# Performance work log

Measured on AMD Instinct MI355X. Metric: run time of the kernel, lower is better.

## Reference

```python
import jax, jax.numpy as jnp
import numpy as np

N_CHARS, EMB, HID, SEQ = 256, 512, 2048, 8192


def setup_inputs() -> dict:
    key = jax.random.key(0)
    ks = jax.random.split(key, 12)
    s = 0.02
    cat = EMB + HID
    return {
        "input_seq": jax.random.randint(ks[0], (SEQ,), 0, N_CHARS, dtype=jnp.int32),
        "hidden": jnp.zeros((HID,), jnp.float32),
        "cell": jnp.zeros((HID,), jnp.float32),
        "embedding": jax.random.normal(ks[1], (N_CHARS, EMB), jnp.float32) * s,
        "Wf": jax.random.normal(ks[2], (HID, cat), jnp.float32) * s,
        "bf": jax.random.normal(ks[3], (HID,), jnp.float32) * s,
        "Wi": jax.random.normal(ks[4], (HID, cat), jnp.float32) * s,
        "bi": jax.random.normal(ks[5], (HID,), jnp.float32) * s,
        "Wo": jax.random.normal(ks[6], (HID, cat), jnp.float32) * s,
        "bo": jax.random.normal(ks[7], (HID,), jnp.float32) * s,
        "Wc": jax.random.normal(ks[8], (HID, cat), jnp.float32) * s,
        "bc": jax.random.normal(ks[9], (HID,), jnp.float32) * s,
        "Wout": jax.random.normal(ks[10], (N_CHARS, HID), jnp.float32) * s,
        "bout": jax.random.normal(ks[11], (N_CHARS,), jnp.float32) * s,
    }


def reference(input_seq, hidden, cell, embedding, Wf, bf, Wi, bi, Wo, bo, Wc, bc, Wout, bout):
    def step(carry, idx):
        h, c = carry
        x = embedding[idx]                       # [EMB]
        z = jnp.concatenate([x, h])              # [EMB+HID], order matches torch concat([i, h])
        f = jax.nn.sigmoid(Wf @ z + bf)
        i = jax.nn.sigmoid(Wi @ z + bi)
        o = jax.nn.sigmoid(Wo @ z + bo)
        c_tilde = jnp.tanh(Wc @ z + bc)
        c_new = f * c + i * c_tilde
        h_new = o * jnp.tanh(c_new)
        pred = Wout @ h_new + bout               # [N_CHARS]
        return (h_new, c_new), pred

    (h, c), outs = jax.lax.scan(step, (hidden, cell), input_seq)
    return outs, h, c  # outs: [SEQ, N_CHARS]
```

## Files before the change

### kernel.cpp

```cpp
#include <hip/hip_runtime.h>
#include <cstdint>
#include <cstddef>

#define SEQ   8192
#define EMB   512
#define HID   2048
#define NCH   256
#define CAT   (EMB + HID)
#define NBLK  256
#define NTH   512
#define NROW  8192

typedef unsigned int u32x4 __attribute__((ext_vector_type(4)));

__device__ __forceinline__ unsigned long long packpair(float v, unsigned tag) {
    return ((unsigned long long)tag << 32) | (unsigned long long)__float_as_uint(v);
}

__device__ __forceinline__ float fast_sig(float x) {
    return __builtin_amdgcn_rcpf(1.f + __expf(-x));
}
__device__ __forceinline__ float fast_tanh(float x) {
    return 1.f - 2.f * __builtin_amdgcn_rcpf(__expf(2.f * x) + 1.f);
}

#define DPP_ADD(x, ctrl) \
    x += __int_as_float(__builtin_amdgcn_update_dpp(0, __float_as_int(x), ctrl, 0xF, 0xF, true))

__device__ __forceinline__ float wave_sum(float x) {
    DPP_ADD(x, 0x111);
    DPP_ADD(x, 0x112);
    DPP_ADD(x, 0x114);
    DPP_ADD(x, 0x118);
    x += __shfl_xor(x, 16, 64);
    x += __shfl_xor(x, 32, 64);
    return x;
}

#define ST4(N0,N1,N2,N3, V) asm volatile( \
    "v_accvgpr_write_b32 a" #N0 ", %0\n\t" \
    "v_accvgpr_write_b32 a" #N1 ", %1\n\t" \
    "v_accvgpr_write_b32 a" #N2 ", %2\n\t" \
    "v_accvgpr_write_b32 a" #N3 ", %3" \
    :: "v"((V).x), "v"((V).y), "v"((V).z), "v"((V).w) \
    : "a" #N0, "a" #N1, "a" #N2, "a" #N3)

#define DOT16(A0,A1,A2,A3, B0,B1,B2,B3, C0,C1,C2,C3, D0,D1,D2,D3, Z0,Z1,Z2,Z3) \
    "v_accvgpr_read_b32 v68, a" #A0 "\n\t" \
    "v_accvgpr_read_b32 v69, a" #B0 "\n\t" \
    "v_accvgpr_read_b32 v70, a" #C0 "\n\t" \
    "v_accvgpr_read_b32 v71, a" #D0 "\n\t" \
    "v_fmac_f32 %0, v68, " Z0 "\n\t" \
    "v_accvgpr_read_b32 v68, a" #A1 "\n\t" \
    "v_fmac_f32 %1, v69, " Z0 "\n\t" \
    "v_accvgpr_read_b32 v69, a" #B1 "\n\t" \
    "v_fmac_f32 %2, v70, " Z0 "\n\t" \
    "v_accvgpr_read_b32 v70, a" #C1 "\n\t" \
    "v_fmac_f32 %3, v71, " Z0 "\n\t" \
    "v_accvgpr_read_b32 v71, a" #D1 "\n\t" \
    "v_fmac_f32 %0, v68, " Z1 "\n\t" \
    "v_accvgpr_read_b32 v68, a" #A2 "\n\t" \
    "v_fmac_f32 %1, v69, " Z1 "\n\t" \
    "v_accvgpr_read_b32 v69, a" #B2 "\n\t" \
    "v_fmac_f32 %2, v70, " Z1 "\n\t" \
    "v_accvgpr_read_b32 v70, a" #C2 "\n\t" \
    "v_fmac_f32 %3, v71, " Z1 "\n\t" \
    "v_accvgpr_read_b32 v71, a" #D2 "\n\t" \
    "v_fmac_f32 %0, v68, " Z2 "\n\t" \
    "v_accvgpr_read_b32 v68, a" #A3 "\n\t" \
    "v_fmac_f32 %1, v69, " Z2 "\n\t" \
    "v_accvgpr_read_b32 v69, a" #B3 "\n\t" \
    "v_fmac_f32 %2, v70, " Z2 "\n\t" \
    "v_accvgpr_read_b32 v70, a" #C3 "\n\t" \
    "v_fmac_f32 %3, v71, " Z2 "\n\t" \
    "v_accvgpr_read_b32 v71, a" #D3 "\n\t" \
    "v_fmac_f32 %0, v68, " Z3 "\n\t" \
    "v_fmac_f32 %1, v69, " Z3 "\n\t" \
    "v_fmac_f32 %2, v70, " Z3 "\n\t" \
    "v_fmac_f32 %3, v71, " Z3 "\n\t"

#define ACLOB \
    "a0","a1","a2","a3","a4","a5","a6","a7","a8","a9", \
    "a10","a11","a12","a13","a14","a15","a16","a17","a18","a19", \
    "a20","a21","a22","a23","a24","a25","a26","a27","a28","a29", \
    "a30","a31","a32","a33","a34","a35","a36","a37","a38","a39", \
    "a40","a41","a42","a43","a44","a45","a46","a47","a48","a49", \
    "a50","a51","a52","a53","a54","a55","a56","a57","a58","a59", \
    "a60","a61","a62","a63","a64","a65","a66","a67","a68","a69", \
    "a70","a71","a72","a73","a74","a75","a76","a77","a78","a79", \
    "a80","a81","a82","a83","a84","a85","a86","a87","a88","a89", \
    "a90","a91","a92","a93","a94","a95","a96","a97","a98","a99", \
    "a100","a101","a102","a103","a104","a105","a106","a107","a108","a109", \
    "a110","a111","a112","a113","a114","a115","a116","a117","a118","a119", \
    "a120","a121","a122","a123","a124","a125","a126","a127"
#define VCLOB \
    "v60","v61","v62","v63","v64","v65","v66","v67","v68","v69","v70","v71"

__global__ __launch_bounds__(256)
void build_ptab(const float* __restrict__ emb,
                const float* __restrict__ Wf, const float* __restrict__ Wi,
                const float* __restrict__ Wo, const float* __restrict__ Wc,
                const float* __restrict__ bfv, const float* __restrict__ biv,
                const float* __restrict__ bov, const float* __restrict__ bcv,
                float* __restrict__ P)
{
    const int r = blockIdx.x;
    const int j = r >> 2, g = r & 3;
    const float* W = (g == 0 ? Wf : g == 1 ? Wi : g == 2 ? Wo : Wc) + (size_t)j * CAT;
    const float  b = (g == 0 ? bfv : g == 1 ? biv : g == 2 ? bov : bcv)[j];
    const float* x = emb + (size_t)threadIdx.x * EMB;
    float acc = 0.f;
    #pragma unroll 8
    for (int k = 0; k < EMB; k += 4) {
        const float4 w4 = *(const float4*)(W + k);
        const float4 x4 = *(const float4*)(x + k);
        acc = fmaf(w4.x, x4.x, acc); acc = fmaf(w4.y, x4.y, acc);
        acc = fmaf(w4.z, x4.z, acc); acc = fmaf(w4.w, x4.w, acc);
    }
    P[((size_t)threadIdx.x << 13) + r] = acc + b;
}

__global__
__attribute__((amdgpu_flat_work_group_size(NTH, NTH)))
__attribute__((amdgpu_waves_per_eu(2, 2)))
void lstm_persistent(const int* __restrict__ seq,
                     const float* __restrict__ h0,
                     const float* __restrict__ c0,
                     const float* __restrict__ Wf, const float* __restrict__ Wi,
                     const float* __restrict__ Wo, const float* __restrict__ Wc,
                     const float* __restrict__ Wout, const float* __restrict__ boutv,
                     const float* __restrict__ Ptab,
                     float* __restrict__ out,
                     unsigned long long* __restrict__ hbuf)
{
    const int cu  = blockIdx.x;
    const int tid = threadIdx.x;
    const int wv  = tid >> 6;
    const int ln  = tid & 63;
    const int j   = cu * 8 + wv;

    __shared__ float z_lds[HID];
    __shared__ float wred[8];
    __shared__ float hpub[8];

    {
        const float* r0 = Wf + (size_t)j * CAT + EMB + 4 * ln;
        const float* r1 = Wi + (size_t)j * CAT + EMB + 4 * ln;
        const float* r2 = Wo + (size_t)j * CAT + EMB + 4 * ln;
        const float* r3 = Wc + (size_t)j * CAT + EMB + 4 * ln;
        float4 v;
        v = *(const float4*)(r0 +    0); ST4(0,1,2,3, v);
        v = *(const float4*)(r0 +  256); ST4(4,5,6,7, v);
        v = *(const float4*)(r0 +  512); ST4(8,9,10,11, v);
        v = *(const float4*)(r0 +  768); ST4(12,13,14,15, v);
        v = *(const float4*)(r0 + 1024); ST4(16,17,18,19, v);
        v = *(const float4*)(r0 + 1280); ST4(20,21,22,23, v);
        v = *(const float4*)(r0 + 1536); ST4(24,25,26,27, v);
        v = *(const float4*)(r0 + 1792); ST4(28,29,30,31, v);
        v = *(const float4*)(r1 +    0); ST4(32,33,34,35, v);
        v = *(const float4*)(r1 +  256); ST4(36,37,38,39, v);
        v = *(const float4*)(r1 +  512); ST4(40,41,42,43, v);
        v = *(const float4*)(r1 +  768); ST4(44,45,46,47, v);
        v = *(const float4*)(r1 + 1024); ST4(48,49,50,51, v);
        v = *(const float4*)(r1 + 1280); ST4(52,53,54,55, v);
        v = *(const float4*)(r1 + 1536); ST4(56,57,58,59, v);
        v = *(const float4*)(r1 + 1792); ST4(60,61,62,63, v);
        v = *(const float4*)(r2 +    0); ST4(64,65,66,67, v);
        v = *(const float4*)(r2 +  256); ST4(68,69,70,71, v);
        v = *(const float4*)(r2 +  512); ST4(72,73,74,75, v);
        v = *(const float4*)(r2 +  768); ST4(76,77,78,79, v);
        v = *(const float4*)(r2 + 1024); ST4(80,81,82,83, v);
        v = *(const float4*)(r2 + 1280); ST4(84,85,86,87, v);
        v = *(const float4*)(r2 + 1536); ST4(88,89,90,91, v);
        v = *(const float4*)(r2 + 1792); ST4(92,93,94,95, v);
        v = *(const float4*)(r3 +    0); ST4(96,97,98,99, v);
        v = *(const float4*)(r3 +  256); ST4(100,101,102,103, v);
        v = *(const float4*)(r3 +  512); ST4(104,105,106,107, v);
        v = *(const float4*)(r3 +  768); ST4(108,109,110,111, v);
        v = *(const float4*)(r3 + 1024); ST4(112,113,114,115, v);
        v = *(const float4*)(r3 + 1280); ST4(116,117,118,119, v);
        v = *(const float4*)(r3 + 1536); ST4(120,121,122,123, v);
        v = *(const float4*)(r3 + 1792); ST4(124,125,126,127, v);
    }
    const float4 ww = *(const float4*)(Wout + (size_t)cu * HID + tid * 4);
    const float bout_cu = boutv[cu];
    const unsigned zaddr = (unsigned)(size_t)&z_lds[4 * ln];

    float c = c0[j];

    if (tid < 8) {
        const int jm = cu * 8 + tid;
        __hip_atomic_store(&hbuf[jm], packpair(h0[jm], 1u),
                           __ATOMIC_RELAXED, __HIP_MEMORY_SCOPE_AGENT);
    }

    int budget = 1 << 22;
    float hv0 = 0.f, hv1 = 0.f, hv2 = 0.f, hv3 = 0.f;
    int ch = seq[0];

    #pragma unroll 1
    for (int t = 0; t < SEQ; ++t) {
        int chv = ch;
        asm volatile("" : "+v"(chv));
        const float4 p4 = *(const float4*)(Ptab + ((size_t)(unsigned)chv << 13) + (j << 2));
        if (t + 1 < SEQ) ch = seq[t + 1];

        {
            const unsigned long long* p = hbuf + (size_t)(t & 1) * HID + tid * 4;
            const unsigned want = (unsigned)(t + 1);
            u32x4 q0 = {0,0,0,0}, q1 = {0,0,0,0};
            while (true) {
                unsigned long long s0;
                asm volatile(
                    "global_load_dwordx2 %0, %1, off sc0 sc1\n\t"
                    "s_waitcnt vmcnt(0)"
                    : "=v"(s0) : "v"(p) : "memory");
                if ((unsigned)(s0 >> 32) == want) {
                    asm volatile(
                        "global_load_dwordx4 %0, %2, off sc0 sc1\n\t"
                        "global_load_dwordx4 %1, %3, off sc0 sc1\n\t"
                        "s_waitcnt vmcnt(0)"
                        : "=&v"(q0), "=&v"(q1)
                        : "v"(p), "v"(p + 2)
                        : "memory");
                    if (q0.y == want && q0.w == want &&
                        q1.y == want && q1.w == want) break;
                }
                if (--budget < 0) break;
                __builtin_amdgcn_s_sleep(1);
            }
            hv0 = __uint_as_float(q0.x);
            hv1 = __uint_as_float(q0.z);
            hv2 = __uint_as_float(q1.x);
            hv3 = __uint_as_float(q1.z);
        }
        *(float4*)&z_lds[tid * 4] = make_float4(hv0, hv1, hv2, hv3);
        __syncthreads();

        float ac0 = 0.f, ac1 = 0.f, ac2 = 0.f, ac3 = 0.f;
        asm volatile(
            "s_waitcnt lgkmcnt(0)\n\t"
            "ds_read_b128 v[60:63], %[za] offset:0\n\t"
            "ds_read_b128 v[64:67], %[za] offset:1024\n\t"
            "s_waitcnt lgkmcnt(1)\n\t"
            DOT16(0,1,2,3, 32,33,34,35, 64,65,66,67, 96,97,98,99, "v60","v61","v62","v63")
            "ds_read_b128 v[60:63], %[za] offset:2048\n\t"
            "s_waitcnt lgkmcnt(1)\n\t"
            DOT16(4,5,6,7, 36,37,38,39, 68,69,70,71, 100,101,102,103, "v64","v65","v66","v67")
            "ds_read_b128 v[64:67], %[za] offset:3072\n\t"
            "s_waitcnt lgkmcnt(1)\n\t"
            DOT16(8,9,10,11, 40,41,42,43, 72,73,74,75, 104,105,106,107, "v60","v61","v62","v63")
            "ds_read_b128 v[60:63], %[za] offset:4096\n\t"
            "s_waitcnt lgkmcnt(1)\n\t"
            DOT16(12,13,14,15, 44,45,46,47, 76,77,78,79, 108,109,110,111, "v64","v65","v66","v67")
            "ds_read_b128 v[64:67], %[za] offset:5120\n\t"
            "s_waitcnt lgkmcnt(1)\n\t"
            DOT16(16,17,18,19, 48,49,50,51, 80,81,82,83, 112,113,114,115, "v60","v61","v62","v63")
            "ds_read_b128 v[60:63], %[za] offset:6144\n\t"
            "s_waitcnt lgkmcnt(1)\n\t"
            DOT16(20,21,22,23, 52,53,54,55, 84,85,86,87, 116,117,118,119, "v64","v65","v66","v67")
            "ds_read_b128 v[64:67], %[za] offset:7168\n\t"
            "s_waitcnt lgkmcnt(1)\n\t"
            DOT16(24,25,26,27, 56,57,58,59, 88,89,90,91, 120,121,122,123, "v60","v61","v62","v63")
            "s_waitcnt lgkmcnt(0)\n\t"
            DOT16(28,29,30,31, 60,61,62,63, 92,93,94,95, 124,125,126,127, "v64","v65","v66","v67")
            : "+v"(ac0), "+v"(ac1), "+v"(ac2), "+v"(ac3)
            : [za] "v"(zaddr)
            : ACLOB, VCLOB, "memory");

        float aw = fmaf(ww.x, hv0, fmaf(ww.y, hv1, fmaf(ww.z, hv2, ww.w * hv3)));

        ac0 = wave_sum(ac0); ac1 = wave_sum(ac1);
        ac2 = wave_sum(ac2); ac3 = wave_sum(ac3);
        aw  = wave_sum(aw);

        if (ln == 63) {
            const float gf = fast_sig(ac0 + p4.x);
            const float gi = fast_sig(ac1 + p4.y);
            const float go = fast_sig(ac2 + p4.z);
            const float ct = fast_tanh(ac3 + p4.w);
            c = fmaf(gf, c, gi * ct);
            hpub[wv] = go * fast_tanh(c);
            wred[wv] = aw;
        }
        __syncthreads();
        if (tid < 8) {
            __hip_atomic_store(&hbuf[(size_t)((t + 1) & 1) * HID + cu * 8 + tid],
                               packpair(hpub[tid], (unsigned)(t + 2)),
                               __ATOMIC_RELAXED, __HIP_MEMORY_SCOPE_AGENT);
        }
        if (tid == NTH - 1 && t >= 1) {
            float s = bout_cu;
            #pragma unroll
            for (int q = 0; q < 8; ++q) s += wred[q];
            out[(size_t)(t - 1) * NCH + cu] = s;
        }
    }

    {
        const unsigned long long* p = hbuf + (size_t)(SEQ & 1) * HID + tid * 4;
        const unsigned want = (unsigned)(SEQ + 1);
        u32x4 q0 = {0,0,0,0}, q1 = {0,0,0,0};
        while (true) {
            unsigned long long s0;
            asm volatile(
                "global_load_dwordx2 %0, %1, off sc0 sc1\n\t"
                "s_waitcnt vmcnt(0)"
                : "=v"(s0) : "v"(p) : "memory");
            if ((unsigned)(s0 >> 32) == want) {
                asm volatile(
                    "global_load_dwordx4 %0, %2, off sc0 sc1\n\t"
                    "global_load_dwordx4 %1, %3, off sc0 sc1\n\t"
                    "s_waitcnt vmcnt(0)"
                    : "=&v"(q0), "=&v"(q1)
                    : "v"(p), "v"(p + 2)
                    : "memory");
                if (q0.y == want && q0.w == want &&
                    q1.y == want && q1.w == want) break;
            }
            if (--budget < 0) break;
            __builtin_amdgcn_s_sleep(1);
        }
        hv0 = __uint_as_float(q0.x);
        hv1 = __uint_as_float(q0.z);
        hv2 = __uint_as_float(q1.x);
        hv3 = __uint_as_float(q1.z);

        float aw = fmaf(ww.x, hv0, fmaf(ww.y, hv1, fmaf(ww.z, hv2, ww.w * hv3)));
        aw = wave_sum(aw);
        if (ln == 63) wred[wv] = aw;
        __syncthreads();
        if (tid == NTH - 1) {
            float s = bout_cu;
            #pragma unroll
            for (int q = 0; q < 8; ++q) s += wred[q];
            out[(size_t)(SEQ - 1) * NCH + cu] = s;
        }
        if (cu == 0) {
            *(float4*)&out[(size_t)SEQ * NCH + tid * 4] =
                make_float4(hv0, hv1, hv2, hv3);
        }
        if (ln == 63) out[(size_t)SEQ * NCH + HID + j] = c;
    }
}

extern "C" void kernel_launch(void* const* d_in, const int* in_sizes, int n_in,
                              void* d_out, int out_size, void* d_ws, size_t ws_size,
                              hipStream_t stream)
{
    const int*   seq  = (const int*)  d_in[0];
    const float* h0   = (const float*)d_in[1];
    const float* c0   = (const float*)d_in[2];
    const float* emb  = (const float*)d_in[3];
    const float* Wf   = (const float*)d_in[4];
    const float* bf_  = (const float*)d_in[5];
    const float* Wi   = (const float*)d_in[6];
    const float* bi_  = (const float*)d_in[7];
    const float* Wo   = (const float*)d_in[8];
    const float* bo_  = (const float*)d_in[9];
    const float* Wc   = (const float*)d_in[10];
    const float* bc_  = (const float*)d_in[11];
    const float* Wout = (const float*)d_in[12];
    const float* bout = (const float*)d_in[13];
    float* out = (float*)d_out;

    unsigned long long* hbuf = (unsigned long long*)d_ws;
    float* Ptab = (float*)((char*)d_ws + 2 * HID * sizeof(unsigned long long));

    build_ptab<<<dim3(NROW), dim3(256), 0, stream>>>(
        emb, Wf, Wi, Wo, Wc, bf_, bi_, bo_, bc_, Ptab);

    void* args[] = { (void*)&seq, (void*)&h0, (void*)&c0,
                     (void*)&Wf, (void*)&Wi, (void*)&Wo, (void*)&Wc,
                     (void*)&Wout, (void*)&bout, (void*)&Ptab,
                     (void*)&out, (void*)&hbuf };

    hipError_t e = hipLaunchCooperativeKernel((void*)lstm_persistent,
                                              dim3(NBLK), dim3(NTH),
                                              args, 0, stream);
    if (e != hipSuccess) {
        lstm_persistent<<<dim3(NBLK), dim3(NTH), 0, stream>>>(
            seq, h0, c0, Wf, Wi, Wo, Wc, Wout, bout, Ptab, out, hbuf);
    }
}
```

Measured before the change: 23.90 ms.

## Replace per-value tagged h exchange with per-block tag flags plus separate data buffer

Replaces the 64-bit packed value+tag hidden-state exchange with a plain float data buffer and one tag word per block. Only wave 0 polls the 256 tags (4 per lane) and the block then reads the h vector with a single dwordx4 load per thread. Publishers write data, wait for completion, then write the tag. This halves the bytes each thread polls and reads and moves polling to one wave, at the cost of an extra __syncthreads and a store-then-flag serialization step per timestep. Correctness depends on store ordering with sc0 sc1 across the device.

```diff
diff --git a/kernel.cpp b/kernel.cpp
--- a/kernel.cpp
+++ b/kernel.cpp
@@ -12,10 +12,6 @@
 #define NROW  8192
 
 typedef unsigned int u32x4 __attribute__((ext_vector_type(4)));
-
-__device__ __forceinline__ unsigned long long packpair(float v, unsigned tag) {
-    return ((unsigned long long)tag << 32) | (unsigned long long)__float_as_uint(v);
-}
 
 __device__ __forceinline__ float fast_sig(float x) {
     return __builtin_amdgcn_rcpf(1.f + __expf(-x));
@@ -130,8 +126,9 @@
                      const float* __restrict__ Wo, const float* __restrict__ Wc,
                      const float* __restrict__ Wout, const float* __restrict__ boutv,
                      const float* __restrict__ Ptab,
-                     float* __restrict__ out,
-                     unsigned long long* __restrict__ hbuf)
+                     float* __restrict__ hdata,
+                     unsigned* __restrict__ tags,
+                     float* __restrict__ gout)
 {
     const int cu  = blockIdx.x;
     const int tid = threadIdx.x;
@@ -139,9 +136,10 @@
     const int ln  = tid & 63;
     const int j   = cu * 8 + wv;
 
-    __shared__ float z_lds[HID];
+    __shared__ float z[HID];
+    __shared__ float hpub[8];
     __shared__ float wred[8];
-    __shared__ float hpub[8];
+    __shared__ float wfin[8];
 
     {
         const float* r0 = Wf + (size_t)j * CAT + EMB + 4 * ln;
@@ -184,62 +182,73 @@
     }
     const float4 ww = *(const float4*)(Wout + (size_t)cu * HID + tid * 4);
     const float bout_cu = boutv[cu];
-    const unsigned zaddr = (unsigned)(size_t)&z_lds[4 * ln];
 
     float c = c0[j];
 
-    if (tid < 8) {
-        const int jm = cu * 8 + tid;
-        __hip_atomic_store(&hbuf[jm], packpair(h0[jm], 1u),
-                           __ATOMIC_RELAXED, __HIP_MEMORY_SCOPE_AGENT);
+    if (wv == 0) {
+        const int idx = cu * 8 + (ln & 7);
+        const unsigned du = __float_as_uint(h0[idx]);
+        const float* daddr = hdata + idx;
+        if (ln < 8)
+            asm volatile("global_store_dword %0, %1, off sc0 sc1"
+                         :: "v"(daddr), "v"(du) : "memory");
+        asm volatile("s_waitcnt vmcnt(0)" ::: "memory");
+        if (ln == 0) {
+            const unsigned* taddr = tags + cu;
+            asm volatile("global_store_dword %0, %1, off sc0 sc1"
+                         :: "v"(taddr), "v"(1u) : "memory");
+        }
     }
 
     int budget = 1 << 22;
     float hv0 = 0.f, hv1 = 0.f, hv2 = 0.f, hv3 = 0.f;
     int ch = seq[0];
+    const unsigned zaddr = (unsigned)(size_t)&z[4 * ln];
 
     #pragma unroll 1
     for (int t = 0; t < SEQ; ++t) {
+        const int par = t & 1;
+        const unsigned want = (unsigned)(t + 1);
+
         int chv = ch;
         asm volatile("" : "+v"(chv));
         const float4 p4 = *(const float4*)(Ptab + ((size_t)(unsigned)chv << 13) + (j << 2));
         if (t + 1 < SEQ) ch = seq[t + 1];
 
-        {
-            const unsigned long long* p = hbuf + (size_t)(t & 1) * HID + tid * 4;
-            const unsigned want = (unsigned)(t + 1);
-            u32x4 q0 = {0,0,0,0}, q1 = {0,0,0,0};
+        if (wv == 0) {
+            const unsigned* taddr = tags + par * NCH + 4 * ln;
             while (true) {
-                unsigned long long s0;
+                u32x4 tg;
                 asm volatile(
-                    "global_load_dwordx2 %0, %1, off sc0 sc1\n\t"
+                    "global_load_dwordx4 %0, %1, off sc0 sc1\n\t"
                     "s_waitcnt vmcnt(0)"
-                    : "=v"(s0) : "v"(p) : "memory");
-                if ((unsigned)(s0 >> 32) == want) {
-                    asm volatile(
-                        "global_load_dwordx4 %0, %2, off sc0 sc1\n\t"
-                        "global_load_dwordx4 %1, %3, off sc0 sc1\n\t"
-                        "s_waitcnt vmcnt(0)"
-                        : "=&v"(q0), "=&v"(q1)
-                        : "v"(p), "v"(p + 2)
-                        : "memory");
-                    if (q0.y == want && q0.w == want &&
-                        q1.y == want && q1.w == want) break;
-                }
+                    : "=v"(tg) : "v"(taddr) : "memory");
+                const int ok = (tg.x == want) & (tg.y == want) &
+                               (tg.z == want) & (tg.w == want);
+                if (__all(ok)) break;
                 if (--budget < 0) break;
                 __builtin_amdgcn_s_sleep(1);
             }
-            hv0 = __uint_as_float(q0.x);
-            hv1 = __uint_as_float(q0.z);
-            hv2 = __uint_as_float(q1.x);
-            hv3 = __uint_as_float(q1.z);
-        }
-        *(float4*)&z_lds[tid * 4] = make_float4(hv0, hv1, hv2, hv3);
+        }
+        __syncthreads();
+
+        {
+            const float* hp = hdata + (size_t)par * HID + 4 * tid;
+            u32x4 hq;
+            asm volatile(
+                "global_load_dwordx4 %0, %1, off sc0 sc1\n\t"
+                "s_waitcnt vmcnt(0)"
+                : "=v"(hq) : "v"(hp) : "memory");
+            hv0 = __uint_as_float(hq.x);
+            hv1 = __uint_as_float(hq.y);
+            hv2 = __uint_as_float(hq.z);
+            hv3 = __uint_as_float(hq.w);
+        }
+        *(float4*)&z[4 * tid] = make_float4(hv0, hv1, hv2, hv3);
         __syncthreads();
 
         float ac0 = 0.f, ac1 = 0.f, ac2 = 0.f, ac3 = 0.f;
         asm volatile(
-            "s_waitcnt lgkmcnt(0)\n\t"
             "ds_read_b128 v[60:63], %[za] offset:0\n\t"
             "ds_read_b128 v[64:67], %[za] offset:1024\n\t"
             "s_waitcnt lgkmcnt(1)\n\t"
@@ -284,63 +293,77 @@
             wred[wv] = aw;
         }
         __syncthreads();
-        if (tid < 8) {
-            __hip_atomic_store(&hbuf[(size_t)((t + 1) & 1) * HID + cu * 8 + tid],
-                               packpair(hpub[tid], (unsigned)(t + 2)),
-                               __ATOMIC_RELAXED, __HIP_MEMORY_SCOPE_AGENT);
+
+        if (wv == 0) {
+            const int par2 = (t + 1) & 1;
+            const unsigned du = __float_as_uint(hpub[ln & 7]);
+            const float* daddr = hdata + (size_t)par2 * HID + cu * 8 + (ln & 7);
+            if (ln < 8)
+                asm volatile("global_store_dword %0, %1, off sc0 sc1"
+                             :: "v"(daddr), "v"(du) : "memory");
+            asm volatile("s_waitcnt vmcnt(0)" ::: "memory");
+            if (ln == 0) {
+                const unsigned* taddr = tags + par2 * NCH + cu;
+                const unsigned tv = (unsigned)(t + 2);
+                asm volatile("global_store_dword %0, %1, off sc0 sc1"
+                             :: "v"(taddr), "v"(tv) : "memory");
+            }
         }
         if (tid == NTH - 1 && t >= 1) {
             float s = bout_cu;
             #pragma unroll
             for (int q = 0; q < 8; ++q) s += wred[q];
-            out[(size_t)(t - 1) * NCH + cu] = s;
+            gout[(size_t)(t - 1) * NCH + cu] = s;
         }
     }
 
     {
-        const unsigned long long* p = hbuf + (size_t)(SEQ & 1) * HID + tid * 4;
+        const int par = SEQ & 1;
         const unsigned want = (unsigned)(SEQ + 1);
-        u32x4 q0 = {0,0,0,0}, q1 = {0,0,0,0};
-        while (true) {
-            unsigned long long s0;
+        if (wv == 0) {
+            const unsigned* taddr = tags + par * NCH + 4 * ln;
+            while (true) {
+                u32x4 tg;
+                asm volatile(
+                    "global_load_dwordx4 %0, %1, off sc0 sc1\n\t"
+                    "s_waitcnt vmcnt(0)"
+                    : "=v"(tg) : "v"(taddr) : "memory");
+                const int ok = (tg.x == want) & (tg.y == want) &
+                               (tg.z == want) & (tg.w == want);
+                if (__all(ok)) break;
+                if (--budget < 0) break;
+                __builtin_amdgcn_s_sleep(1);
+            }
+        }
+        __syncthreads();
+        {
+            const float* hp = hdata + (size_t)par * HID + 4 * tid;
+            u32x4 hq;
             asm volatile(
-                "global_load_dwordx2 %0, %1, off sc0 sc1\n\t"
+                "global_load_dwordx4 %0, %1, off sc0 sc1\n\t"
                 "s_waitcnt vmcnt(0)"
-                : "=v"(s0) : "v"(p) : "memory");
-            if ((unsigned)(s0 >> 32) == want) {
-                asm volatile(
-                    "global_load_dwordx4 %0, %2, off sc0 sc1\n\t"
-                    "global_load_dwordx4 %1, %3, off sc0 sc1\n\t"
-                    "s_waitcnt vmcnt(0)"
-                    : "=&v"(q0), "=&v"(q1)
-                    : "v"(p), "v"(p + 2)
-                    : "memory");
-                if (q0.y == want && q0.w == want &&
-                    q1.y == want && q1.w == want) break;
-            }
-            if (--budget < 0) break;
-            __builtin_amdgcn_s_sleep(1);
-        }
-        hv0 = __uint_as_float(q0.x);
-        hv1 = __uint_as_float(q0.z);
-        hv2 = __uint_as_float(q1.x);
-        hv3 = __uint_as_float(q1.z);
+                : "=v"(hq) : "v"(hp) : "memory");
+            hv0 = __uint_as_float(hq.x);
+            hv1 = __uint_as_float(hq.y);
+            hv2 = __uint_as_float(hq.z);
+            hv3 = __uint_as_float(hq.w);
+        }
 
         float aw = fmaf(ww.x, hv0, fmaf(ww.y, hv1, fmaf(ww.z, hv2, ww.w * hv3)));
         aw = wave_sum(aw);
-        if (ln == 63) wred[wv] = aw;
+        if (ln == 63) wfin[wv] = aw;
         __syncthreads();
         if (tid == NTH - 1) {
             float s = bout_cu;
             #pragma unroll
-            for (int q = 0; q < 8; ++q) s += wred[q];
-            out[(size_t)(SEQ - 1) * NCH + cu] = s;
+            for (int q = 0; q < 8; ++q) s += wfin[q];
+            gout[(size_t)(SEQ - 1) * NCH + cu] = s;
         }
         if (cu == 0) {
-            *(float4*)&out[(size_t)SEQ * NCH + tid * 4] =
+            *(float4*)&gout[(size_t)SEQ * NCH + tid * 4] =
                 make_float4(hv0, hv1, hv2, hv3);
         }
-        if (ln == 63) out[(size_t)SEQ * NCH + HID + j] = c;
+        if (ln == 63) gout[(size_t)SEQ * NCH + HID + j] = c;
     }
 }
 
@@ -364,8 +387,9 @@
     const float* bout = (const float*)d_in[13];
     float* out = (float*)d_out;
 
-    unsigned long long* hbuf = (unsigned long long*)d_ws;
-    float* Ptab = (float*)((char*)d_ws + 2 * HID * sizeof(unsigned long long));
+    float*    hdata = (float*)d_ws;
+    unsigned* tags  = (unsigned*)((char*)d_ws + 16 * 1024);
+    float*    Ptab  = (float*)((char*)d_ws + 32 * 1024);
 
     build_ptab<<<dim3(NROW), dim3(256), 0, stream>>>(
         emb, Wf, Wi, Wo, Wc, bf_, bi_, bo_, bc_, Ptab);
@@ -373,13 +397,13 @@
     void* args[] = { (void*)&seq, (void*)&h0, (void*)&c0,
                      (void*)&Wf, (void*)&Wi, (void*)&Wo, (void*)&Wc,
                      (void*)&Wout, (void*)&bout, (void*)&Ptab,
-                     (void*)&out, (void*)&hbuf };
+                     (void*)&hdata, (void*)&tags, (void*)&out };
 
     hipError_t e = hipLaunchCooperativeKernel((void*)lstm_persistent,
                                               dim3(NBLK), dim3(NTH),
                                               args, 0, stream);
     if (e != hipSuccess) {
         lstm_persistent<<<dim3(NBLK), dim3(NTH), 0, stream>>>(
-            seq, h0, c0, Wf, Wi, Wo, Wc, Wout, bout, Ptab, out, hbuf);
-    }
-}
+            seq, h0, c0, Wf, Wi, Wo, Wc, Wout, bout, Ptab, hdata, tags, out);
+    }
+}
```

Result: slower. 26.83 ms (+12.2%).
